# Optimization experiments

Hardware: AMD Instinct MI355X
Metric: run time of the kernel (lower is better)

## Reference

```python
import jax, jax.numpy as jnp
import numpy as np
import math

B, C, H, W = 16, 512, 32, 32
GROUPS = 32
EPS = 1e-5


def group_norm(x, w, b):
    # x: [B, C, H, W]; normalize within each of GROUPS channel groups over (C//G, H, W)
    Bx, Cx, Hx, Wx = x.shape
    xg = x.reshape(Bx, GROUPS, Cx // GROUPS, Hx, Wx)
    mean = xg.mean(axis=(2, 3, 4), keepdims=True)
    var = xg.var(axis=(2, 3, 4), keepdims=True)
    xg = (xg - mean) * jax.lax.rsqrt(var + EPS)
    xn = xg.reshape(Bx, Cx, Hx, Wx)
    return xn * w[None, :, None, None] + b[None, :, None, None]


def setup_inputs() -> dict:
    key = jax.random.key(0)
    ks = jax.random.split(key, 4)
    x = jax.random.normal(ks[0], (B, C, H, W), dtype=jnp.float32)
    gn_w = jnp.ones((C,), dtype=jnp.float32)
    gn_b = jnp.zeros((C,), dtype=jnp.float32)
    # Conv2d 1x1 weights as [out, in] matrices; PyTorch default init scale
    qkv_w = jax.random.normal(ks[1], (3 * C, C), dtype=jnp.float32) * (1.0 / math.sqrt(C))
    qkv_b = jnp.zeros((3 * C,), dtype=jnp.float32)
    out_w = jax.random.normal(ks[2], (C, C), dtype=jnp.float32) * (1.0 / math.sqrt(C))
    out_b = jnp.zeros((C,), dtype=jnp.float32)
    return {"x": x, "gn_w": gn_w, "gn_b": gn_b, "qkv_w": qkv_w,
            "qkv_b": qkv_b, "out_w": out_w, "out_b": out_b}


def reference(x, gn_w, gn_b, qkv_w, qkv_b, out_w, out_b):
    Bx, Cx, Hx, Wx = x.shape
    N = Hx * Wx
    h = group_norm(x, gn_w, gn_b)                       # [B, C, H, W]
    hf = h.reshape(Bx, Cx, N)                           # [B, C, N]
    # 1x1 conv == channel matmul
    qkv = jnp.einsum('oc,bcn->bon', qkv_w, hf) + qkv_b[None, :, None]  # [B, 3C, N]
    q, k, v = jnp.split(qkv, 3, axis=1)                 # each [B, C, N]
    q = q.transpose(0, 2, 1)                            # [B, N, C]
    v = v.transpose(0, 2, 1)                            # [B, N, C]
    scale = 1.0 / math.sqrt(Cx)
    attn = jnp.einsum('bnc,bcm->bnm', q, k) * scale     # [B, N, N]
    attn = jax.nn.softmax(attn, axis=-1)
    o = jnp.einsum('bnm,bmc->bnc', attn, v)             # [B, N, C]
    o = o.transpose(0, 2, 1)                            # [B, C, N]
    o = jnp.einsum('oc,bcn->bon', out_w, o) + out_b[None, :, None]
    return x + o.reshape(Bx, Cx, Hx, Wx)
```

## Files before the change

### kernel.cpp

```cpp
#include <hip/hip_runtime.h>

typedef unsigned short u16;
typedef short short8 __attribute__((ext_vector_type(8)));
typedef float floatx4 __attribute__((ext_vector_type(4)));
typedef u16 u16x4 __attribute__((ext_vector_type(4)));
typedef u16 u16x8 __attribute__((ext_vector_type(8)));

#define DEVI __device__ __forceinline__

DEVI u16 f2bf(float x) {
    union { float f; unsigned u; } c; c.f = x;
    unsigned u = c.u;
    u += 0x7fffu + ((u >> 16) & 1u);
    return (u16)(u >> 16);
}
DEVI u16 f2bf_fast(float x) {
    union { float f; unsigned u; } c; c.f = x;
    return (u16)((c.u + 0x8000u) >> 16);
}
DEVI float bf2f(u16 h) {
    union { unsigned u; float f; } c; c.u = ((unsigned)h) << 16;
    return c.f;
}

DEVI void gload_lds16(const void* g, void* l) {
    auto gp = (const __attribute__((address_space(1))) unsigned*)(unsigned long long)g;
    auto lp = (__attribute__((address_space(3))) unsigned*)(unsigned)(unsigned long long)l;
    __builtin_amdgcn_global_load_lds(gp, lp, 16, 0, 0);
}

__global__ __launch_bounds__(256) void gn_fused_kernel(const float* __restrict__ x,
                                                       const float* __restrict__ w,
                                                       const float* __restrict__ bb,
                                                       u16* __restrict__ h) {
    const int bg = blockIdx.x;
    const int b = bg >> 5, g = bg & 31;
    const float* xg = x + (long long)bg * 16384;
    const int n0 = threadIdx.x * 4;

    float4 xv[16];
    float s = 0.f, s2 = 0.f;
    #pragma unroll
    for (int cc = 0; cc < 16; cc++) {
        xv[cc] = *(const float4*)&xg[cc * 1024 + n0];
        s  += xv[cc].x + xv[cc].y + xv[cc].z + xv[cc].w;
        s2 += xv[cc].x*xv[cc].x + xv[cc].y*xv[cc].y + xv[cc].z*xv[cc].z + xv[cc].w*xv[cc].w;
    }
    #pragma unroll
    for (int m = 1; m < 64; m <<= 1) { s += __shfl_xor(s, m, 64); s2 += __shfl_xor(s2, m, 64); }
    __shared__ float rs[4], rq[4];
    if ((threadIdx.x & 63) == 0) { rs[threadIdx.x >> 6] = s; rq[threadIdx.x >> 6] = s2; }
    __syncthreads();
    float mean = (rs[0] + rs[1] + rs[2] + rs[3]) * (1.f / 16384.f);
    float var  = (rq[0] + rq[1] + rq[2] + rq[3]) * (1.f / 16384.f) - mean * mean;
    float rstd = rsqrtf(var + 1e-5f);

    u16x8 o[4][2];
    #pragma unroll
    for (int cc = 0; cc < 16; cc++) {
        int c = g * 16 + cc;
        float sc = w[c] * rstd;
        float sh = bb[c] - mean * sc;
        o[0][cc >> 3][cc & 7] = f2bf(xv[cc].x * sc + sh);
        o[1][cc >> 3][cc & 7] = f2bf(xv[cc].y * sc + sh);
        o[2][cc >> 3][cc & 7] = f2bf(xv[cc].z * sc + sh);
        o[3][cc >> 3][cc & 7] = f2bf(xv[cc].w * sc + sh);
    }
    u16* hb = h + ((long long)b * 1024 + n0) * 512 + g * 16;
    #pragma unroll
    for (int k = 0; k < 4; k++) {
        *(u16x8*)&hb[(long long)k * 512]     = o[k][0];
        *(u16x8*)&hb[(long long)k * 512 + 8] = o[k][1];
    }
}

__global__ __launch_bounds__(256) void wconv_kernel(const float* __restrict__ w1, u16* __restrict__ o1,
                                                    const float* __restrict__ w2, u16* __restrict__ o2) {
    int i = blockIdx.x * 256 + threadIdx.x;
    const float* src; u16* dst; int j;
    if (i < 196608) { src = w1; dst = o1; j = i; }
    else            { src = w2; dst = o2; j = i - 196608; }
    float4 v = *(const float4*)&src[j * 4];
    u16x4 p; p[0] = f2bf(v.x); p[1] = f2bf(v.y); p[2] = f2bf(v.z); p[3] = f2bf(v.w);
    *(u16x4*)&dst[j * 4] = p;
}

__global__ __launch_bounds__(256) void lreduce_kernel(const float* __restrict__ ps,
                                                      float* __restrict__ invl) {
    int i = blockIdx.x * 256 + threadIdx.x;
    int z = i >> 10, n = i & 1023;
    float l = 0.f;
    #pragma unroll
    for (int kb = 0; kb < 8; kb++) l += ps[((z * 8 + kb) << 10) + n];
    invl[i] = 1.f / l;
}

template <int MODE, int NX, int NY, bool STATS>
__global__ __launch_bounds__(256, 3)
void gemm_bt_kernel(const u16* __restrict__ A, const u16* __restrict__ Bt,
                    void* __restrict__ C0,
                    const float* __restrict__ bias, const float* __restrict__ res,
                    float* __restrict__ aux,
                    float scale, int lda, int ldb, int ldc,
                    long long sA, long long sB, long long sC, long long sR, int K) {
    int bx, by, bz;
    if (NX > 0) {
        const int lid  = blockIdx.x;
        const int xcd  = lid & 7;
        const int slot = lid >> 3;
        const int per  = NX * NY;
        const int j    = slot / per;
        const int w    = slot - j * per;
        bz = xcd + 8 * j;
        bx = w % NX;
        by = w / NX;
    } else {
        bx = blockIdx.x; by = blockIdx.y; bz = blockIdx.z;
    }
    const int t    = threadIdx.x;
    const int lane = t & 63;
    const int wave = t >> 6;
    const int m0   = by * 128;
    const int n0   = bx * 128;
    A  += (long long)bz * sA;
    Bt += (long long)bz * sB;

    __shared__ __align__(16) u16 smem[16384];
    u16* As = smem;
    u16* Bs = smem + 8192;

    const int wm = wave >> 1, wn = wave & 1;
    const int quad = lane >> 4, lrow = lane & 15;

    floatx4 acc[4][4];
    #pragma unroll
    for (int i = 0; i < 4; i++)
        #pragma unroll
        for (int j = 0; j < 4; j++)
            #pragma unroll
            for (int r = 0; r < 4; r++) acc[i][j][r] = 0.f;

    const int rowA = t >> 2;
    const int kch  = (t & 3) * 8;
    const u16* Ag = A  + (long long)(m0 + rowA) * lda + kch;
    const u16* Bg = Bt + (long long)(n0 + rowA) * ldb + kch;
    u16* Al = &As[t * 8];
    u16* Bl = &Bs[t * 8];
    const long long a64 = (long long)64 * lda;
    const long long b64 = (long long)64 * ldb;
    const u16* Bg3 = Bt + (long long)n0 * ldb;

    for (int k0 = 0; k0 < K; k0 += 64) {
        gload_lds16(Ag + k0,            Al);
        gload_lds16(Ag + k0 + a64,      Al + 2048);
        gload_lds16(Ag + k0 + 32,       Al + 4096);
        gload_lds16(Ag + k0 + 32 + a64, Al + 6144);
        if (MODE != 3) {
            gload_lds16(Bg + k0,            Bl);
            gload_lds16(Bg + k0 + b64,      Bl + 2048);
            gload_lds16(Bg + k0 + 32,       Bl + 4096);
            gload_lds16(Bg + k0 + 32 + b64, Bl + 6144);
        } else {
            #pragma unroll
            for (int q = 0; q < 4; q++) {
                const int row = ((q & 1) ? 64 : 0) + (t >> 2);
                const int kc  = (q >> 1) * 32 + (t & 3) * 8;
                u16x8 sv = *(const u16x8*)&Bg3[(long long)row * ldb + k0 + kc];
                u16x8 ev;
                #pragma unroll
                for (int e = 0; e < 8; e++)
                    ev[e] = f2bf_fast(__expf(bf2f(sv[e])));
                *(u16x8*)&Bs[q * 2048 + t * 8] = ev;
            }
        }
        __syncthreads();
        #pragma unroll
        for (int kk = 0; kk < 2; kk++) {
            short8 af[4], bfr[4];
            #pragma unroll
            for (int i = 0; i < 4; i++)
                af[i] = *(const short8*)&As[kk*4096 + (wm*64 + i*16 + lrow)*32 + quad*8];
            #pragma unroll
            for (int j = 0; j < 4; j++)
                bfr[j] = *(const short8*)&Bs[kk*4096 + (wn*64 + j*16 + lrow)*32 + quad*8];
            #pragma unroll
            for (int i = 0; i < 4; i++)
                #pragma unroll
                for (int j = 0; j < 4; j++)
                    acc[i][j] = __builtin_amdgcn_mfma_f32_16x16x32_bf16(af[i], bfr[j], acc[i][j], 0, 0, 0);
        }
        __syncthreads();
    }

    const int ST = 136;

    if (MODE == 1) {
        #pragma unroll
        for (int p = 0; p < 4; p++) {
            if (p) __syncthreads();
            if (wm == (p >> 1)) {
                #pragma unroll
                for (int ii = 0; ii < 2; ii++) {
                    const int i = (p & 1) * 2 + ii;
                    const int row = ii * 16 + quad * 4;
                    #pragma unroll
                    for (int j = 0; j < 4; j++) {
                        const int cB = wn * 64 + j * 16 + lrow;
                        #pragma unroll
                        for (int r = 0; r < 4; r++)
                            smem[(row + r) * ST + cB] = f2bf(acc[i][j][r] * scale);
                    }
                }
            }
            __syncthreads();
            const int rr = t >> 3, cc = (t & 7) * 16;
            u16x8 a0 = *(u16x8*)&smem[rr * ST + cc];
            u16x8 a1 = *(u16x8*)&smem[rr * ST + cc + 8];
            u16* Cp = (u16*)C0 + (long long)bz * sC + (long long)(m0 + p * 32 + rr) * ldc + n0 + cc;
            *(u16x8*)Cp = a0;
            *(u16x8*)(Cp + 8) = a1;
            if (STATS) {
                float ls = 0.f;
                #pragma unroll
                for (int e = 0; e < 8; e++)
                    ls += __expf(bf2f(a0[e])) + __expf(bf2f(a1[e]));
                #pragma unroll
                for (int m2 = 1; m2 < 8; m2 <<= 1) ls += __shfl_xor(ls, m2, 8);
                if ((t & 7) == 0)
                    aux[((long long)(bz * 8 + bx)) * 1024 + m0 + p * 32 + rr] = ls;
            }
        }
    } else if (MODE == 2) {
        #pragma unroll
        for (int p = 0; p < 4; p++) {
            if (p) __syncthreads();
            if (wn == (p >> 1)) {
                #pragma unroll
                for (int jj = 0; jj < 2; jj++) {
                    const int j = (p & 1) * 2 + jj;
                    const int row = jj * 16 + lrow;
                    #pragma unroll
                    for (int i = 0; i < 4; i++) {
                        const int mmL = wm * 64 + i * 16 + quad * 4;
                        u16x4 pk;
                        #pragma unroll
                        for (int r = 0; r < 4; r++)
                            pk[r] = f2bf(acc[i][j][r] + bias[m0 + mmL + r]);
                        *(u16x4*)&smem[row * ST + mmL] = pk;
                    }
                }
            }
            __syncthreads();
            const int rr = t >> 3, cc = (t & 7) * 16;
            u16x8 a0 = *(u16x8*)&smem[rr * ST + cc];
            u16x8 a1 = *(u16x8*)&smem[rr * ST + cc + 8];
            u16* Cp = (u16*)C0 + (long long)(n0 + p * 32 + rr) * ldc + m0 + cc;
            *(u16x8*)Cp = a0;
            *(u16x8*)(Cp + 8) = a1;
        }
    } else {
        float* smf = (float*)smem;
        const int SF = 132;
        float* C = (float*)C0 + (long long)bz * sC;
        const float* rz = res + (long long)bz * sR;
        const float* il = aux + (long long)bz * 1024;
        #pragma unroll
        for (int p = 0; p < 8; p++) {
            if (p) __syncthreads();
            if (wm == (p >> 2)) {
                const int i = p & 3;
                #pragma unroll
                for (int j = 0; j < 4; j++) {
                    const int cB = wn * 64 + j * 16 + lrow;
                    #pragma unroll
                    for (int r = 0; r < 4; r++)
                        smf[(quad * 4 + r) * SF + cB] = acc[i][j][r];
                }
            }
            __syncthreads();
            const int rr = t >> 4, cc = (t & 15) * 8;
            const float bsv = bias[m0 + p * 16 + rr];
            float4 il0 = *(const float4*)&il[n0 + cc];
            float4 il1 = *(const float4*)&il[n0 + cc + 4];
            const long long gro = (long long)(m0 + p * 16 + rr) * ldc + n0 + cc;
            float4 rv0 = *(const float4*)&rz[gro];
            float4 rv1 = *(const float4*)&rz[gro + 4];
            float4 ov0, ov1;
            ov0.x = smf[rr*SF + cc + 0] * il0.x + bsv + rv0.x;
            ov0.y = smf[rr*SF + cc + 1] * il0.y + bsv + rv0.y;
            ov0.z = smf[rr*SF + cc + 2] * il0.z + bsv + rv0.z;
            ov0.w = smf[rr*SF + cc + 3] * il0.w + bsv + rv0.w;
            ov1.x = smf[rr*SF + cc + 4] * il1.x + bsv + rv1.x;
            ov1.y = smf[rr*SF + cc + 5] * il1.y + bsv + rv1.y;
            ov1.z = smf[rr*SF + cc + 6] * il1.z + bsv + rv1.z;
            ov1.w = smf[rr*SF + cc + 7] * il1.w + bsv + rv1.w;
            *(float4*)&C[gro]     = ov0;
            *(float4*)&C[gro + 4] = ov1;
        }
    }
}

extern "C" void kernel_launch(void* const* d_in, const int* in_sizes, int n_in,
                              void* d_out, int out_size, void* d_ws, size_t ws_size,
                              hipStream_t stream) {
    (void)in_sizes; (void)n_in; (void)out_size; (void)ws_size;
    const float* x     = (const float*)d_in[0];
    const float* gn_w  = (const float*)d_in[1];
    const float* gn_b  = (const float*)d_in[2];
    const float* qkv_w = (const float*)d_in[3];
    const float* qkv_b = (const float*)d_in[4];
    const float* out_w = (const float*)d_in[5];
    const float* out_b = (const float*)d_in[6];
    float* out = (float*)d_out;

    char* ws = (char*)d_ws;
    u16*  h_t   = (u16*)ws;  ws += (size_t)16*1024*512*2;
    u16*  qkv_t = (u16*)ws;  ws += (size_t)16*1024*1536*2;
    u16*  vprm  = (u16*)ws;  ws += (size_t)512*16384*2;
    u16*  S     = (u16*)ws;  ws += (size_t)16*1024*1024*2;
    u16*  wq    = (u16*)ws;  ws += (size_t)1536*512*2;
    u16*  wo    = (u16*)ws;  ws += (size_t)512*512*2;
    float* psum = (float*)ws; ws += (size_t)16*8*1024*4;
    float* invl = (float*)ws; ws += (size_t)16*1024*4;

    wconv_kernel<<<1024, 256, 0, stream>>>(qkv_w, wq, out_w, wo);
    gn_fused_kernel<<<512, 256, 0, stream>>>(x, gn_w, gn_b, h_t);

    gemm_bt_kernel<2, 0, 0, false><<<dim3(128, 12, 1), 256, 0, stream>>>(
        wq, h_t, qkv_t, qkv_b, nullptr, nullptr, 1.0f,
        512, 512, 1536, 0, 0, 0, 0, 512);

    gemm_bt_kernel<1, 0, 0, false><<<dim3(128, 4, 1), 256, 0, stream>>>(
        wo, qkv_t + 1024, vprm, nullptr, nullptr, nullptr, 1.0f,
        512, 1536, 16384, 0, 0, 0, 0, 512);

    gemm_bt_kernel<1, 8, 8, true><<<1024, 256, 0, stream>>>(
        qkv_t, qkv_t + 512, S, nullptr, nullptr, psum, 0.044194173824159216f,
        1536, 1536, 1024,
        (long long)1024*1536, (long long)1024*1536, (long long)1024*1024, 0, 512);

    lreduce_kernel<<<64, 256, 0, stream>>>(psum, invl);

    gemm_bt_kernel<3, 8, 4, false><<<512, 256, 0, stream>>>(
        vprm, S, out, out_b, x, invl, 1.0f,
        16384, 1024, 1024,
        1024, (long long)1024*1024, (long long)512*1024, (long long)512*1024, 1024);
}
```

Measured before the change: 209.0 us.

## Fold V projection into output weights and move exp into QK epilogue

Precomputes Wo·Wv as a small bf16 matrix plus a bias vector Wo·bv, so the Wo-projected V comes straight from the normalized input. This drops the V slice from the QKV GEMM and shrinks the qkv buffer. Exponentials are now applied once in the QK^T epilogue, storing exp(S) and summing it directly, instead of being recomputed in every PV tile load. Occupancy hint raised to 4 blocks per CU. Risks: an extra bf16 rounding of the fused weight, exp without max subtraction, and possible register spills.

```diff
diff --git a/kernel.cpp b/kernel.cpp
--- a/kernel.cpp
+++ b/kernel.cpp
@@ -13,10 +13,6 @@
     unsigned u = c.u;
     u += 0x7fffu + ((u >> 16) & 1u);
     return (u16)(u >> 16);
-}
-DEVI u16 f2bf_fast(float x) {
-    union { float f; unsigned u; } c; c.f = x;
-    return (u16)((c.u + 0x8000u) >> 16);
 }
 DEVI float bf2f(u16 h) {
     union { unsigned u; float f; } c; c.u = ((unsigned)h) << 16;
@@ -75,14 +71,40 @@
 }
 
 __global__ __launch_bounds__(256) void wconv_kernel(const float* __restrict__ w1, u16* __restrict__ o1,
-                                                    const float* __restrict__ w2, u16* __restrict__ o2) {
+                                                    const float* __restrict__ w2, u16* __restrict__ o2,
+                                                    u16* __restrict__ wvT) {
     int i = blockIdx.x * 256 + threadIdx.x;
     const float* src; u16* dst; int j;
-    if (i < 196608) { src = w1; dst = o1; j = i; }
-    else            { src = w2; dst = o2; j = i - 196608; }
+    bool isw1 = i < 196608;
+    if (isw1) { src = w1; dst = o1; j = i; }
+    else      { src = w2; dst = o2; j = i - 196608; }
     float4 v = *(const float4*)&src[j * 4];
     u16x4 p; p[0] = f2bf(v.x); p[1] = f2bf(v.y); p[2] = f2bf(v.z); p[3] = f2bf(v.w);
     *(u16x4*)&dst[j * 4] = p;
+    if (isw1 && j >= 131072) {
+        int e4 = j * 4;
+        int vc = (e4 >> 9) - 1024;
+        int ci = e4 & 511;
+        wvT[(ci + 0) * 512 + vc] = p[0];
+        wvT[(ci + 1) * 512 + vc] = p[1];
+        wvT[(ci + 2) * 512 + vc] = p[2];
+        wvT[(ci + 3) * 512 + vc] = p[3];
+    }
+}
+
+__global__ __launch_bounds__(256) void dvec_kernel(const float* __restrict__ wo,
+                                                   const float* __restrict__ qb,
+                                                   float* __restrict__ d) {
+    int o = blockIdx.x * 256 + threadIdx.x;
+    const float4* r = (const float4*)(wo + (long long)o * 512);
+    const float4* b = (const float4*)(qb + 1024);
+    float s = 0.f;
+    #pragma unroll 4
+    for (int c = 0; c < 128; c++) {
+        float4 a = r[c], q = b[c];
+        s += a.x*q.x + a.y*q.y + a.z*q.z + a.w*q.w;
+    }
+    d[o] = s;
 }
 
 __global__ __launch_bounds__(256) void lreduce_kernel(const float* __restrict__ ps,
@@ -96,7 +118,7 @@
 }
 
 template <int MODE, int NX, int NY, bool STATS>
-__global__ __launch_bounds__(256, 3)
+__global__ __launch_bounds__(256, 4)
 void gemm_bt_kernel(const u16* __restrict__ A, const u16* __restrict__ Bt,
                     void* __restrict__ C0,
                     const float* __restrict__ bias, const float* __restrict__ res,
@@ -148,31 +170,16 @@
     u16* Bl = &Bs[t * 8];
     const long long a64 = (long long)64 * lda;
     const long long b64 = (long long)64 * ldb;
-    const u16* Bg3 = Bt + (long long)n0 * ldb;
 
     for (int k0 = 0; k0 < K; k0 += 64) {
         gload_lds16(Ag + k0,            Al);
         gload_lds16(Ag + k0 + a64,      Al + 2048);
         gload_lds16(Ag + k0 + 32,       Al + 4096);
         gload_lds16(Ag + k0 + 32 + a64, Al + 6144);
-        if (MODE != 3) {
-            gload_lds16(Bg + k0,            Bl);
-            gload_lds16(Bg + k0 + b64,      Bl + 2048);
-            gload_lds16(Bg + k0 + 32,       Bl + 4096);
-            gload_lds16(Bg + k0 + 32 + b64, Bl + 6144);
-        } else {
-            #pragma unroll
-            for (int q = 0; q < 4; q++) {
-                const int row = ((q & 1) ? 64 : 0) + (t >> 2);
-                const int kc  = (q >> 1) * 32 + (t & 3) * 8;
-                u16x8 sv = *(const u16x8*)&Bg3[(long long)row * ldb + k0 + kc];
-                u16x8 ev;
-                #pragma unroll
-                for (int e = 0; e < 8; e++)
-                    ev[e] = f2bf_fast(__expf(bf2f(sv[e])));
-                *(u16x8*)&Bs[q * 2048 + t * 8] = ev;
-            }
-        }
+        gload_lds16(Bg + k0,            Bl);
+        gload_lds16(Bg + k0 + b64,      Bl + 2048);
+        gload_lds16(Bg + k0 + 32,       Bl + 4096);
+        gload_lds16(Bg + k0 + 32 + b64, Bl + 6144);
         __syncthreads();
         #pragma unroll
         for (int kk = 0; kk < 2; kk++) {
@@ -207,8 +214,12 @@
                     for (int j = 0; j < 4; j++) {
                         const int cB = wn * 64 + j * 16 + lrow;
                         #pragma unroll
-                        for (int r = 0; r < 4; r++)
-                            smem[(row + r) * ST + cB] = f2bf(acc[i][j][r] * scale);
+                        for (int r = 0; r < 4; r++) {
+                            float v = acc[i][j][r] * scale;
+                            if (STATS) v = __expf(v);
+                            else if (bias) v += bias[m0 + p * 32 + row + r];
+                            smem[(row + r) * ST + cB] = f2bf(v);
+                        }
                     }
                 }
             }
@@ -223,7 +234,7 @@
                 float ls = 0.f;
                 #pragma unroll
                 for (int e = 0; e < 8; e++)
-                    ls += __expf(bf2f(a0[e])) + __expf(bf2f(a1[e]));
+                    ls += bf2f(a0[e]) + bf2f(a1[e]);
                 #pragma unroll
                 for (int m2 = 1; m2 < 8; m2 <<= 1) ls += __shfl_xor(ls, m2, 8);
                 if ((t & 7) == 0)
@@ -315,34 +326,42 @@
 
     char* ws = (char*)d_ws;
     u16*  h_t   = (u16*)ws;  ws += (size_t)16*1024*512*2;
-    u16*  qkv_t = (u16*)ws;  ws += (size_t)16*1024*1536*2;
+    u16*  qkv_t = (u16*)ws;  ws += (size_t)16*1024*1024*2;
     u16*  vprm  = (u16*)ws;  ws += (size_t)512*16384*2;
-    u16*  S     = (u16*)ws;  ws += (size_t)16*1024*1024*2;
-    u16*  wq    = (u16*)ws;  ws += (size_t)1536*512*2;
-    u16*  wo    = (u16*)ws;  ws += (size_t)512*512*2;
+    u16*  E     = (u16*)ws;  ws += (size_t)16*1024*1024*2;
+    u16*  wqb   = (u16*)ws;  ws += (size_t)1536*512*2;
+    u16*  wob   = (u16*)ws;  ws += (size_t)512*512*2;
+    u16*  wvT   = (u16*)ws;  ws += (size_t)512*512*2;
+    u16*  wprm  = (u16*)ws;  ws += (size_t)512*512*2;
+    float* dv   = (float*)ws; ws += (size_t)512*4;
     float* psum = (float*)ws; ws += (size_t)16*8*1024*4;
     float* invl = (float*)ws; ws += (size_t)16*1024*4;
 
-    wconv_kernel<<<1024, 256, 0, stream>>>(qkv_w, wq, out_w, wo);
+    wconv_kernel<<<1024, 256, 0, stream>>>(qkv_w, wqb, out_w, wob, wvT);
+    dvec_kernel<<<2, 256, 0, stream>>>(out_w, qkv_b, dv);
     gn_fused_kernel<<<512, 256, 0, stream>>>(x, gn_w, gn_b, h_t);
 
-    gemm_bt_kernel<2, 0, 0, false><<<dim3(128, 12, 1), 256, 0, stream>>>(
-        wq, h_t, qkv_t, qkv_b, nullptr, nullptr, 1.0f,
-        512, 512, 1536, 0, 0, 0, 0, 512);
+    gemm_bt_kernel<1, 0, 0, false><<<dim3(4, 4, 1), 256, 0, stream>>>(
+        wob, wvT, wprm, nullptr, nullptr, nullptr, 1.0f,
+        512, 512, 512, 0, 0, 0, 0, 512);
+
+    gemm_bt_kernel<2, 0, 0, false><<<dim3(128, 8, 1), 256, 0, stream>>>(
+        wqb, h_t, qkv_t, qkv_b, nullptr, nullptr, 1.0f,
+        512, 512, 1024, 0, 0, 0, 0, 512);
 
     gemm_bt_kernel<1, 0, 0, false><<<dim3(128, 4, 1), 256, 0, stream>>>(
-        wo, qkv_t + 1024, vprm, nullptr, nullptr, nullptr, 1.0f,
-        512, 1536, 16384, 0, 0, 0, 0, 512);
+        wprm, h_t, vprm, dv, nullptr, nullptr, 1.0f,
+        512, 512, 16384, 0, 0, 0, 0, 512);
 
     gemm_bt_kernel<1, 8, 8, true><<<1024, 256, 0, stream>>>(
-        qkv_t, qkv_t + 512, S, nullptr, nullptr, psum, 0.044194173824159216f,
-        1536, 1536, 1024,
-        (long long)1024*1536, (long long)1024*1536, (long long)1024*1024, 0, 512);
+        qkv_t, qkv_t + 512, E, nullptr, nullptr, psum, 0.044194173824159216f,
+        1024, 1024, 1024,
+        (long long)1024*1024, (long long)1024*1024, (long long)1024*1024, 0, 512);
 
     lreduce_kernel<<<64, 256, 0, stream>>>(psum, invl);
 
     gemm_bt_kernel<3, 8, 4, false><<<512, 256, 0, stream>>>(
-        vprm, S, out, out_b, x, invl, 1.0f,
+        vprm, E, out, out_b, x, invl, 1.0f,
         16384, 1024, 1024,
         1024, (long long)1024*1024, (long long)512*1024, (long long)512*1024, 1024);
 }
```

New measurement: 238.8 us. 1.14x slower.
